# Optimization experiments

Hardware: AMD Instinct MI355X
Metric: run time of the kernel (lower is better)

The kernel has to match this reference:

```python
import jax, jax.numpy as jnp
import numpy as np
import math

B, S, E = 2, 2048, 1024
H, HD = 16, 64
FF = 4 * E
EPS = float(jnp.finfo(jnp.float32).eps)  # torch nn.RMSNorm default eps


def setup_inputs() -> dict:
    key = jax.random.key(0)
    ks = jax.random.split(key, 20)
    sd = 0.02
    inp = {
        "x": jax.random.normal(ks[0], (B, S, E), jnp.float32),
        "wq": jax.random.normal(ks[1], (E, H * HD), jnp.float32) * sd,
        "bq": jnp.zeros((H * HD,), jnp.float32),
        "wk": jax.random.normal(ks[2], (E, HD), jnp.float32) * sd,
        "bk": jnp.zeros((HD,), jnp.float32),
        "wv": jax.random.normal(ks[3], (E, HD), jnp.float32) * sd,
        "bv": jnp.zeros((HD,), jnp.float32),
        "wo": jax.random.normal(ks[4], (H * HD, E), jnp.float32) * sd,
        "bo": jnp.zeros((E,), jnp.float32),
        "wg": jax.random.normal(ks[5], (E, FF), jnp.float32) * sd,
        "bg": jnp.zeros((FF,), jnp.float32),
        "wu": jax.random.normal(ks[6], (E, FF), jnp.float32) * sd,
        "bu": jnp.zeros((FF,), jnp.float32),
        "wd": jax.random.normal(ks[7], (FF, E), jnp.float32) * sd,
        "bd": jnp.zeros((E,), jnp.float32),
        "g1": jnp.ones((E,), jnp.float32),
        "g2": jnp.ones((E,), jnp.float32),
    }
    return inp


def rmsnorm(x, g):
    ms = jnp.mean(jnp.square(x), axis=-1, keepdims=True)
    return x * jax.lax.rsqrt(ms + EPS) * g


def apply_rope(t):
    # t: [B, H, S, D]; llama-style rotate-half, theta=10000, start_pos=0
    d = t.shape[-1]
    half = d // 2
    inv_freq = 1.0 / (10000.0 ** (jnp.arange(half, dtype=jnp.float32) / half))
    pos = jnp.arange(t.shape[2], dtype=jnp.float32)
    ang = pos[:, None] * inv_freq[None, :]  # [S, half]
    cos, sin = jnp.cos(ang), jnp.sin(ang)
    t1, t2 = t[..., :half], t[..., half:]
    return jnp.concatenate([t1 * cos - t2 * sin, t1 * sin + t2 * cos], axis=-1)


def decoder_fwd(x, wq, bq, wk, bk, wv, bv, wo, bo, wg, bg, wu, bu, wd, bd, g1, g2):
    residual = x
    h = rmsnorm(x, g1)
    # MQA projections: H query heads, 1 shared K/V head
    q = (h @ wq + bq).reshape(B, S, H, HD).transpose(0, 2, 1, 3)  # [B,H,S,D]
    k = (h @ wk + bk)[:, None]                                    # [B,1,S,D]
    v = (h @ wv + bv)                                             # [B,S,D]
    q = apply_rope(q)
    k = apply_rope(k)[:, 0]                                       # [B,S,D]
    scores = jnp.einsum("bhqd,bkd->bhqk", q, k) / math.sqrt(HD)
    causal = jnp.tril(jnp.ones((S, S), dtype=bool))
    scores = jnp.where(causal, scores, -jnp.inf)
    attn = jax.nn.softmax(scores, axis=-1)
    out = jnp.einsum("bhqk,bkd->bhqd", attn, v)
    out = out.transpose(0, 2, 1, 3).reshape(B, S, H * HD)
    x = (out @ wo + bo) + residual
    residual = x
    h = rmsnorm(x, g2)
    gated = jax.nn.gelu(h @ wg + bg, approximate=False)  # torch GELU is exact erf
    up = h @ wu + bu
    x = (up * gated) @ wd + bd
    return x + residual


def reference(x, wq, bq, wk, bk, wv, bv, wo, bo, wg, bg, wu, bu, wd, bd, g1, g2):
    return decoder_fwd(x, wq, bq, wk, bk, wv, bv, wo, bo, wg, bg, wu, bu, wd, bd, g1, g2)
```

## Files before the change

### kernel.cpp

```cpp
#include <hip/hip_runtime.h>
#include <hip/hip_bf16.h>
#include <math.h>

#define BB 2
#define SS 2048
#define EE 1024
#define HH 16
#define HD 64
#define FFF 4096
#define MROWS (BB * SS)
#define EPS_F 1.1920929e-7f
#define NQKV 1152

typedef __hip_bfloat16 bf16;
typedef __attribute__((ext_vector_type(8))) short short8;
typedef __attribute__((ext_vector_type(4))) short short4v;
typedef __attribute__((ext_vector_type(4))) float floatx4;

typedef const __attribute__((address_space(1))) void* gas_t;
typedef __attribute__((address_space(3))) void* las_t;

__global__ __launch_bounds__(256) void rmsnorm_kernel(const float* __restrict__ x,
                                                      const float* __restrict__ g,
                                                      bf16* __restrict__ out,
                                                      int cols) {
    int row = blockIdx.x;
    const float* xr = x + (size_t)row * cols;
    float ss = 0.0f;
    for (int c = threadIdx.x; c < cols; c += 256) {
        float v = xr[c];
        ss += v * v;
    }
    for (int off = 32; off > 0; off >>= 1) ss += __shfl_xor(ss, off, 64);
    __shared__ float red[4];
    int wave = threadIdx.x >> 6;
    if ((threadIdx.x & 63) == 0) red[wave] = ss;
    __syncthreads();
    float tot = red[0] + red[1] + red[2] + red[3];
    float rs = rsqrtf(tot / (float)cols + EPS_F);
    bf16* orow = out + (size_t)row * cols;
    for (int c = threadIdx.x; c < cols; c += 256) {
        orow[c] = __float2bfloat16(xr[c] * rs * g[c]);
    }
}

__global__ __launch_bounds__(256) void transpose_cast_kernel(const float* __restrict__ W,
                                                             bf16* __restrict__ Wt,
                                                             int K, int N) {
    __shared__ float t[32][33];
    int n0 = blockIdx.x * 32, k0 = blockIdx.y * 32;
    int tx = threadIdx.x & 31, ty = threadIdx.x >> 5;
#pragma unroll
    for (int i = 0; i < 4; ++i) {
        int kk = ty + i * 8;
        t[kk][tx] = W[(size_t)(k0 + kk) * N + n0 + tx];
    }
    __syncthreads();
#pragma unroll
    for (int i = 0; i < 4; ++i) {
        int nn = ty + i * 8;
        Wt[(size_t)(n0 + nn) * K + k0 + tx] = __float2bfloat16(t[tx][nn]);
    }
}

__global__ __launch_bounds__(256) void pack_bqkv_kernel(const float* __restrict__ bq,
                                                        const float* __restrict__ bk,
                                                        const float* __restrict__ bv,
                                                        float* __restrict__ bqkv) {
    int t = blockIdx.x * 256 + threadIdx.x;
    if (t >= NQKV) return;
    float v;
    if (t < 1024)      v = bq[t];
    else if (t < 1088) v = bk[t - 1024];
    else               v = bv[t - 1088];
    bqkv[t] = v;
}

#define GK 64

__global__ __launch_bounds__(256) void gemm_qkv_kernel(
        const bf16* __restrict__ A, const bf16* __restrict__ Bt,
        const float* __restrict__ bias,
        bf16* __restrict__ qout, float* __restrict__ kvout, int K) {
    __shared__ short As[128 * GK];
    __shared__ short Bs[128 * GK];
    int tid = threadIdx.x;
    int wave = tid >> 6, lane = tid & 63;
    int wm = (wave >> 1) * 64, wn = (wave & 1) * 64;
    int row0 = blockIdx.y * 128, col0 = blockIdx.x * 128;
    int lr = lane & 15, lq = lane >> 4;

    int srow = wave * 32 + (lane >> 3);
    int scol = (lane & 7) * 8;
    const bf16* Abase = A + (size_t)(row0 + srow) * K + scol;
    const bf16* Bbase = Bt + (size_t)(col0 + srow) * K + scol;

    floatx4 acc[4][4];
#pragma unroll
    for (int mi = 0; mi < 4; ++mi)
#pragma unroll
        for (int ni = 0; ni < 4; ++ni)
            acc[mi][ni] = (floatx4){0.f, 0.f, 0.f, 0.f};

    for (int k0 = 0; k0 < K; k0 += GK) {
        __syncthreads();
#pragma unroll
        for (int c = 0; c < 4; ++c) {
            __builtin_amdgcn_global_load_lds(
                (gas_t)(Abase + (size_t)(c * 8) * K + k0),
                (las_t)&As[(wave * 32 + c * 8) * GK], 16, 0, 0);
            __builtin_amdgcn_global_load_lds(
                (gas_t)(Bbase + (size_t)(c * 8) * K + k0),
                (las_t)&Bs[(wave * 32 + c * 8) * GK], 16, 0, 0);
        }
        __syncthreads();
#pragma unroll
        for (int ks = 0; ks < GK; ks += 32) {
            short8 af[4], bfr[4];
#pragma unroll
            for (int mi = 0; mi < 4; ++mi)
                af[mi] = *(const short8*)&As[(wm + mi * 16 + lr) * GK + ks + lq * 8];
#pragma unroll
            for (int ni = 0; ni < 4; ++ni)
                bfr[ni] = *(const short8*)&Bs[(wn + ni * 16 + lr) * GK + ks + lq * 8];
#pragma unroll
            for (int mi = 0; mi < 4; ++mi)
#pragma unroll
                for (int ni = 0; ni < 4; ++ni)
                    acc[mi][ni] = __builtin_amdgcn_mfma_f32_16x16x32_bf16(
                        af[mi], bfr[ni], acc[mi][ni], 0, 0, 0);
        }
    }

#pragma unroll
    for (int mi = 0; mi < 4; ++mi) {
#pragma unroll
        for (int ni = 0; ni < 4; ++ni) {
            int gc = col0 + wn + ni * 16 + lr;
            float bv = bias[gc];
#pragma unroll
            for (int r = 0; r < 4; ++r) {
                int gr = row0 + wm + mi * 16 + lq * 4 + r;
                float c = acc[mi][ni][r] + bv;
                if (gc < 1024) qout[(size_t)gr * 1024 + gc] = __float2bfloat16(c);
                else           kvout[(size_t)gr * 128 + (gc - 1024)] = c;
            }
        }
    }
}

__global__ __launch_bounds__(256) void gemm_n64_kernel(
        const bf16* __restrict__ A, const bf16* __restrict__ Bt,
        const float* __restrict__ bias, const float* __restrict__ aux,
        float* __restrict__ C, int M, int N, int K) {
    __shared__ short As[128 * GK];
    __shared__ short Bs[64 * GK];
    int tid = threadIdx.x;
    int wave = tid >> 6, lane = tid & 63;
    int wm = wave * 32;
    int row0 = blockIdx.y * 128, col0 = blockIdx.x * 64;
    int lr = lane & 15, lq = lane >> 4;

    int srow = (lane >> 3);
    int scol = (lane & 7) * 8;
    const bf16* Abase = A + (size_t)(row0 + wave * 32 + srow) * K + scol;
    const bf16* Bbase = Bt + (size_t)(col0 + wave * 16 + srow) * K + scol;

    floatx4 acc[2][4];
#pragma unroll
    for (int mi = 0; mi < 2; ++mi)
#pragma unroll
        for (int ni = 0; ni < 4; ++ni)
            acc[mi][ni] = (floatx4){0.f, 0.f, 0.f, 0.f};

    for (int k0 = 0; k0 < K; k0 += GK) {
        __syncthreads();
#pragma unroll
        for (int c = 0; c < 4; ++c)
            __builtin_amdgcn_global_load_lds(
                (gas_t)(Abase + (size_t)(c * 8) * K + k0),
                (las_t)&As[(wave * 32 + c * 8) * GK], 16, 0, 0);
#pragma unroll
        for (int c = 0; c < 2; ++c)
            __builtin_amdgcn_global_load_lds(
                (gas_t)(Bbase + (size_t)(c * 8) * K + k0),
                (las_t)&Bs[(wave * 16 + c * 8) * GK], 16, 0, 0);
        __syncthreads();
#pragma unroll
        for (int ks = 0; ks < GK; ks += 32) {
            short8 af[2], bfr[4];
#pragma unroll
            for (int mi = 0; mi < 2; ++mi)
                af[mi] = *(const short8*)&As[(wm + mi * 16 + lr) * GK + ks + lq * 8];
#pragma unroll
            for (int ni = 0; ni < 4; ++ni)
                bfr[ni] = *(const short8*)&Bs[(ni * 16 + lr) * GK + ks + lq * 8];
#pragma unroll
            for (int mi = 0; mi < 2; ++mi)
#pragma unroll
                for (int ni = 0; ni < 4; ++ni)
                    acc[mi][ni] = __builtin_amdgcn_mfma_f32_16x16x32_bf16(
                        af[mi], bfr[ni], acc[mi][ni], 0, 0, 0);
        }
    }

#pragma unroll
    for (int mi = 0; mi < 2; ++mi) {
#pragma unroll
        for (int ni = 0; ni < 4; ++ni) {
            int gc = col0 + ni * 16 + lr;
            float bv = bias[gc];
#pragma unroll
            for (int r = 0; r < 4; ++r) {
                int gr = row0 + wm + mi * 16 + lq * 4 + r;
                size_t idx = (size_t)gr * N + gc;
                C[idx] = acc[mi][ni][r] + bv + aux[idx];
            }
        }
    }
}

__global__ __launch_bounds__(256, 2) void gemm_ffn_kernel(
        const bf16* __restrict__ A, const bf16* __restrict__ Bg,
        const bf16* __restrict__ Bu, const float* __restrict__ biasg,
        const float* __restrict__ biasu, bf16* __restrict__ C, int K) {
    __shared__ short As[128 * GK];
    __shared__ short Gs[128 * GK];
    __shared__ short Us[128 * GK];
    int tid = threadIdx.x;
    int wave = tid >> 6, lane = tid & 63;
    int wm = (wave >> 1) * 64, wn = (wave & 1) * 64;
    int row0 = blockIdx.y * 128, col0 = blockIdx.x * 128;
    int lr = lane & 15, lq = lane >> 4;

    int srow = wave * 32 + (lane >> 3);
    int scol = (lane & 7) * 8;
    const bf16* Abase = A + (size_t)(row0 + srow) * K + scol;
    const bf16* Gbase = Bg + (size_t)(col0 + srow) * K + scol;
    const bf16* Ubase = Bu + (size_t)(col0 + srow) * K + scol;

    floatx4 ag[4][4], au[4][4];
#pragma unroll
    for (int mi = 0; mi < 4; ++mi)
#pragma unroll
        for (int ni = 0; ni < 4; ++ni) {
            ag[mi][ni] = (floatx4){0.f, 0.f, 0.f, 0.f};
            au[mi][ni] = (floatx4){0.f, 0.f, 0.f, 0.f};
        }

    for (int k0 = 0; k0 < K; k0 += GK) {
        __syncthreads();
#pragma unroll
        for (int c = 0; c < 4; ++c) {
            __builtin_amdgcn_global_load_lds(
                (gas_t)(Abase + (size_t)(c * 8) * K + k0),
                (las_t)&As[(wave * 32 + c * 8) * GK], 16, 0, 0);
            __builtin_amdgcn_global_load_lds(
                (gas_t)(Gbase + (size_t)(c * 8) * K + k0),
                (las_t)&Gs[(wave * 32 + c * 8) * GK], 16, 0, 0);
            __builtin_amdgcn_global_load_lds(
                (gas_t)(Ubase + (size_t)(c * 8) * K + k0),
                (las_t)&Us[(wave * 32 + c * 8) * GK], 16, 0, 0);
        }
        __syncthreads();
#pragma unroll
        for (int ks = 0; ks < GK; ks += 32) {
            short8 af[4], gf[4], uf[4];
#pragma unroll
            for (int mi = 0; mi < 4; ++mi)
                af[mi] = *(const short8*)&As[(wm + mi * 16 + lr) * GK + ks + lq * 8];
#pragma unroll
            for (int ni = 0; ni < 4; ++ni) {
                gf[ni] = *(const short8*)&Gs[(wn + ni * 16 + lr) * GK + ks + lq * 8];
                uf[ni] = *(const short8*)&Us[(wn + ni * 16 + lr) * GK + ks + lq * 8];
            }
#pragma unroll
            for (int mi = 0; mi < 4; ++mi)
#pragma unroll
                for (int ni = 0; ni < 4; ++ni) {
                    ag[mi][ni] = __builtin_amdgcn_mfma_f32_16x16x32_bf16(
                        af[mi], gf[ni], ag[mi][ni], 0, 0, 0);
                    au[mi][ni] = __builtin_amdgcn_mfma_f32_16x16x32_bf16(
                        af[mi], uf[ni], au[mi][ni], 0, 0, 0);
                }
        }
    }

#pragma unroll
    for (int mi = 0; mi < 4; ++mi) {
#pragma unroll
        for (int ni = 0; ni < 4; ++ni) {
            int gc = col0 + wn + ni * 16 + lr;
            float bg_ = biasg[gc], bu_ = biasu[gc];
#pragma unroll
            for (int r = 0; r < 4; ++r) {
                int gr = row0 + wm + mi * 16 + lq * 4 + r;
                float g = ag[mi][ni][r] + bg_;
                float u = au[mi][ni][r] + bu_;
                float v = 0.5f * g * (1.0f + erff(g * 0.70710678118654752f)) * u;
                C[(size_t)gr * FFF + gc] = __float2bfloat16(v);
            }
        }
    }
}

__global__ __launch_bounds__(256) void rope_table_kernel(float* __restrict__ ct,
                                                         float* __restrict__ st) {
    int idx = blockIdx.x * 256 + threadIdx.x;
    int i = idx & 31, s = idx >> 5;
    float inv = powf(10000.0f, -(float)i / 32.0f);
    float ang = (float)s * inv;
    ct[idx] = cosf(ang);
    st[idx] = sinf(ang);
}

__global__ __launch_bounds__(256) void rope_q_kernel(bf16* __restrict__ t,
                                                     const float* __restrict__ ct,
                                                     const float* __restrict__ st,
                                                     int total) {
    int idx = blockIdx.x * 256 + threadIdx.x;
    if (idx >= total) return;
    int i = idx & 31;
    int h = (idx >> 5) % HH;
    int row = idx / (32 * HH);
    int s = row & (SS - 1);
    float c = ct[s * 32 + i];
    float sn = st[s * 32 + i];
    size_t base = (size_t)row * (HH * HD) + h * 64 + i;
    float t1 = (float)t[base];
    float t2 = (float)t[base + 32];
    t[base]      = __float2bfloat16((t1 * c - t2 * sn) * 0.125f);
    t[base + 32] = __float2bfloat16((t1 * sn + t2 * c) * 0.125f);
}

__global__ __launch_bounds__(256) void prep_kv_kernel(const float* __restrict__ kv,
                                                      const float* __restrict__ ct,
                                                      const float* __restrict__ st,
                                                      bf16* __restrict__ kbf,
                                                      bf16* __restrict__ vtb) {
    __shared__ float vt[64][65];
    int s0 = blockIdx.x * 64;
    int b  = blockIdx.y;
    int tid = threadIdx.x;

    for (int i = tid; i < 2048; i += 256) {
        int sl = i >> 5, ii = i & 31;
        int s = s0 + sl;
        size_t base = ((size_t)(b * SS + s)) * 128;
        float k1 = kv[base + ii], k2 = kv[base + ii + 32];
        float c = ct[s * 32 + ii];
        float sn = st[s * 32 + ii];
        size_t ob = ((size_t)(b * SS + s)) * 64;
        kbf[ob + ii]      = __float2bfloat16(k1 * c - k2 * sn);
        kbf[ob + ii + 32] = __float2bfloat16(k1 * sn + k2 * c);
    }

    for (int i = tid; i < 4096; i += 256) {
        int s = i >> 6, d = i & 63;
        vt[d][s] = kv[((size_t)(b * SS + s0 + s)) * 128 + 64 + d];
    }
    __syncthreads();
    for (int i = tid; i < 4096; i += 256) {
        int d = i >> 6, sl = i & 63;
        vtb[((size_t)(b * 64 + d)) * SS + s0 + sl] = __float2bfloat16(vt[d][sl]);
    }
}

#define PST 68
#define SM_SHIFT 6.0f

__global__ __launch_bounds__(256, 3) void attn_mfma_kernel(
        const bf16* __restrict__ q, const bf16* __restrict__ kb,
        const bf16* __restrict__ vt,
        float* __restrict__ O0p, float* __restrict__ O1p,
        float* __restrict__ l0p, float* __restrict__ l1p) {
    __shared__ short Kb_s[2][64 * 64];
    __shared__ short Vb_s[2][64 * 64];
    __shared__ short Ps[4][16 * PST];

    int h = blockIdx.y, b = blockIdx.z;
    int px = blockIdx.x >> 1, half = blockIdx.x & 1;
    int tid = threadIdx.x, w = tid >> 6, lane = tid & 63;
    int lr = lane & 15, quad = lane >> 4;
    int rsw = lane & 7;

    float* __restrict__ Op = half ? O1p : O0p;
    float* __restrict__ lp = half ? l1p : l0p;

    const bf16* kbB = kb + (size_t)b * SS * 64;
    const bf16* vtB = vt + (size_t)b * 64 * SS;

    int st_sub = lane >> 3;
    int st_col = ((lane & 7) ^ st_sub) << 3;

    auto stage_tile = [&](int nxt, int j0s) {
#pragma unroll
        for (int i = 0; i < 2; ++i) {
            int rr = i * 32 + w * 8 + st_sub;
            __builtin_amdgcn_global_load_lds(
                (gas_t)(kbB + (size_t)(j0s + rr) * 64 + st_col),
                (las_t)&Kb_s[nxt][(i * 256 + w * 64) * 8], 16, 0, 0);
            __builtin_amdgcn_global_load_lds(
                (gas_t)(vtB + (size_t)rr * SS + j0s + st_col),
                (las_t)&Vb_s[nxt][(i * 256 + w * 64) * 8], 16, 0, 0);
        }
    };

    for (int pass = 0; pass < 2; ++pass) {
        int qt = (pass == 0) ? px : (SS / 64 - 1 - px);
        int q0 = qt * 64;

        const bf16* qrow = q + ((size_t)(b * SS + q0 + w * 16 + lr)) * (HH * HD) + h * HD;
        short8 qf0 = *(const short8*)(qrow + quad * 8);
        short8 qf1 = *(const short8*)(qrow + 32 + quad * 8);

        int n  = qt + 1;
        int n0 = (n + 1) >> 1;
        int tlo = half ? n0 : 0;
        int thi = half ? n  : n0;

        floatx4 O[4];
#pragma unroll
        for (int ni = 0; ni < 4; ++ni) O[ni] = (floatx4){0.f, 0.f, 0.f, 0.f};
        float lrow[4] = {0.f, 0.f, 0.f, 0.f};

        int cur = 0;
        if (tlo < thi) stage_tile(0, tlo * 64);
        __syncthreads();

        for (int t = tlo; t < thi; ++t) {
            if (t + 1 < thi) stage_tile(cur ^ 1, (t + 1) * 64);

            int j0 = t * 64;

            floatx4 S[4];
#pragma unroll
            for (int ni = 0; ni < 4; ++ni) S[ni] = (floatx4){0.f, 0.f, 0.f, 0.f};
#pragma unroll
            for (int ni = 0; ni < 4; ++ni) {
                const short* Kc = &Kb_s[cur][(ni * 16 + lr) * 64];
                short8 b0 = *(const short8*)&Kc[(quad ^ rsw) * 8];
                short8 b1 = *(const short8*)&Kc[((quad ^ rsw) ^ 4) * 8];
                S[ni] = __builtin_amdgcn_mfma_f32_16x16x32_bf16(qf0, b0, S[ni], 0, 0, 0);
                S[ni] = __builtin_amdgcn_mfma_f32_16x16x32_bf16(qf1, b1, S[ni], 0, 0, 0);
            }

            short8 vf[8];
#pragma unroll
            for (int ni = 0; ni < 4; ++ni) {
                const short* Vc = &Vb_s[cur][(ni * 16 + lr) * 64];
                vf[2 * ni]     = *(const short8*)&Vc[(quad ^ rsw) * 8];
                vf[2 * ni + 1] = *(const short8*)&Vc[((quad ^ rsw) ^ 4) * 8];
            }

            if (t == qt) {
                int rowg = q0 + w * 16 + quad * 4;
#pragma unroll
                for (int ni = 0; ni < 4; ++ni) {
                    int colg = j0 + ni * 16 + lr;
#pragma unroll
                    for (int r = 0; r < 4; ++r)
                        if (colg > rowg + r) S[ni][r] = -3.0e38f;
                }
            }

#pragma unroll
            for (int ni = 0; ni < 4; ++ni)
#pragma unroll
                for (int r = 0; r < 4; ++r)
                    S[ni][r] = __expf(S[ni][r] - SM_SHIFT);
#pragma unroll
            for (int r = 0; r < 4; ++r)
                lrow[r] += S[0][r] + S[1][r] + S[2][r] + S[3][r];

#pragma unroll
            for (int ni = 0; ni < 4; ++ni)
#pragma unroll
                for (int r = 0; r < 4; ++r) {
                    bf16 pb = __float2bfloat16(S[ni][r]);
                    Ps[w][(quad * 4 + r) * PST + ni * 16 + lr] = *(short*)&pb;
                }
            short4v a0 = *(const short4v*)&Ps[w][lr * PST + quad * 8];
            short4v a1 = *(const short4v*)&Ps[w][lr * PST + quad * 8 + 4];
            short4v a2 = *(const short4v*)&Ps[w][lr * PST + 32 + quad * 8];
            short4v a3 = *(const short4v*)&Ps[w][lr * PST + 32 + quad * 8 + 4];
            short8 p0 = __builtin_shufflevector(a0, a1, 0, 1, 2, 3, 4, 5, 6, 7);
            short8 p1 = __builtin_shufflevector(a2, a3, 0, 1, 2, 3, 4, 5, 6, 7);

#pragma unroll
            for (int ni = 0; ni < 4; ++ni) {
                O[ni] = __builtin_amdgcn_mfma_f32_16x16x32_bf16(p0, vf[2 * ni], O[ni], 0, 0, 0);
                O[ni] = __builtin_amdgcn_mfma_f32_16x16x32_bf16(p1, vf[2 * ni + 1], O[ni], 0, 0, 0);
            }

            __syncthreads();
            cur ^= 1;
        }

#pragma unroll
        for (int r = 0; r < 4; ++r) {
            float l = lrow[r];
            for (int off = 1; off < 16; off <<= 1) l += __shfl_xor(l, off, 64);
            lrow[r] = l;
        }

#pragma unroll
        for (int ni = 0; ni < 4; ++ni) {
            int gc = h * 64 + ni * 16 + lr;
#pragma unroll
            for (int r = 0; r < 4; ++r) {
                int gr = b * SS + q0 + w * 16 + quad * 4 + r;
                Op[(size_t)gr * (HH * HD) + gc] = O[ni][r];
            }
        }
        if (lr == 0) {
#pragma unroll
            for (int r = 0; r < 4; ++r) {
                int gr = b * SS + q0 + w * 16 + quad * 4 + r;
                lp[(size_t)gr * HH + h] = lrow[r];
            }
        }
    }
}

__global__ __launch_bounds__(256) void attn_combine_kernel(
        const float* __restrict__ O0p, const float* __restrict__ O1p,
        const float* __restrict__ l0p, const float* __restrict__ l1p,
        bf16* __restrict__ o) {
    int idx = blockIdx.x * 256 + threadIdx.x;
    int d4  = idx & 15;
    int hh  = (idx >> 4) & 15;
    int row = idx >> 8;
    float l = l0p[row * HH + hh] + l1p[row * HH + hh];
    float inv = 1.0f / l;
    size_t base = (size_t)row * (HH * HD) + hh * 64 + d4 * 4;
    float4 a = *(const float4*)(O0p + base);
    float4 c = *(const float4*)(O1p + base);
    short4v o4;
    {
        bf16 v0 = __float2bfloat16((a.x + c.x) * inv);
        bf16 v1 = __float2bfloat16((a.y + c.y) * inv);
        bf16 v2 = __float2bfloat16((a.z + c.z) * inv);
        bf16 v3 = __float2bfloat16((a.w + c.w) * inv);
        o4[0] = *(short*)&v0; o4[1] = *(short*)&v1;
        o4[2] = *(short*)&v2; o4[3] = *(short*)&v3;
    }
    *(short4v*)(o + base) = o4;
}

#define MB (1024ull * 1024ull)

extern "C" void kernel_launch(void* const* d_in, const int* in_sizes, int n_in,
                              void* d_out, int out_size, void* d_ws, size_t ws_size,
                              hipStream_t stream) {
    const float* x  = (const float*)d_in[0];
    const float* wq = (const float*)d_in[1];
    const float* bq = (const float*)d_in[2];
    const float* wk = (const float*)d_in[3];
    const float* bk = (const float*)d_in[4];
    const float* wv = (const float*)d_in[5];
    const float* bv = (const float*)d_in[6];
    const float* wo = (const float*)d_in[7];
    const float* bo = (const float*)d_in[8];
    const float* wg = (const float*)d_in[9];
    const float* bg = (const float*)d_in[10];
    const float* wu = (const float*)d_in[11];
    const float* bu = (const float*)d_in[12];
    const float* wd = (const float*)d_in[13];
    const float* bd = (const float*)d_in[14];
    const float* g1 = (const float*)d_in[15];
    const float* g2 = (const float*)d_in[16];
    float* out = (float*)d_out;

    char* ws = (char*)d_ws;
    bf16*  qbf   = (bf16*)(ws);
    bf16*  wuT   = (bf16*)(ws + 8 * MB);
    float* x2    = (float*)(ws + 16 * MB);
    bf16*  h1b   = (bf16*)(ws + 32 * MB);
    float* kv    = (float*)(ws + 40 * MB);
    bf16*  ao    = (bf16*)(ws + 42 * MB);
    bf16*  gg    = (bf16*)(ws + 50 * MB);
    bf16*  kbf   = (bf16*)(ws + 50 * MB);
    bf16*  vtb   = (bf16*)(ws + 50 * MB + 512 * 1024);
    float* Opart0 = (float*)(ws + 16 * MB);
    float* Opart1 = (float*)(ws + 51 * MB);
    float* lpart0 = (float*)(ws + 67 * MB);
    float* lpart1 = (float*)(ws + 67 * MB + 256 * 1024);
    float* ctab   = (float*)(ws + 68 * MB);
    float* stab   = (float*)(ws + 68 * MB + 256 * 1024);
    bf16*  wqkvT = (bf16*)(ws + 82 * MB);
    float* bqkv  = (float*)(ws + 84 * MB + 512 * 1024);
    bf16*  woT   = (bf16*)(ws + 85 * MB);
    bf16*  wgT   = (bf16*)(ws);
    bf16*  wdT   = (bf16*)(ws + 42 * MB);
    bf16*  h2b   = h1b;

    rmsnorm_kernel<<<MROWS, 256, 0, stream>>>(x, g1, h1b, EE);

    transpose_cast_kernel<<<dim3(EE / 32, EE / 32), 256, 0, stream>>>(wq, wqkvT, EE, EE);
    transpose_cast_kernel<<<dim3(HD / 32, EE / 32), 256, 0, stream>>>(wk, wqkvT + (size_t)1024 * EE, EE, HD);
    transpose_cast_kernel<<<dim3(HD / 32, EE / 32), 256, 0, stream>>>(wv, wqkvT + (size_t)1088 * EE, EE, HD);
    pack_bqkv_kernel<<<(NQKV + 255) / 256, 256, 0, stream>>>(bq, bk, bv, bqkv);
    transpose_cast_kernel<<<dim3(EE / 32, EE / 32), 256, 0, stream>>>(wo, woT, EE, EE);

    gemm_qkv_kernel<<<dim3(NQKV / 128, MROWS / 128), 256, 0, stream>>>(
        h1b, wqkvT, bqkv, qbf, kv, EE);

    rope_table_kernel<<<(SS * 32) / 256, 256, 0, stream>>>(ctab, stab);

    {
        int total_q = MROWS * HH * 32;
        rope_q_kernel<<<(total_q + 255) / 256, 256, 0, stream>>>(qbf, ctab, stab, total_q);
    }
    prep_kv_kernel<<<dim3(SS / 64, BB), 256, 0, stream>>>(kv, ctab, stab, kbf, vtb);

    attn_mfma_kernel<<<dim3(2 * SS / 128, HH, BB), 256, 0, stream>>>(
        qbf, kbf, vtb, Opart0, Opart1, lpart0, lpart1);
    attn_combine_kernel<<<(MROWS * HH * HD / 4) / 256, 256, 0, stream>>>(
        Opart0, Opart1, lpart0, lpart1, ao);

    gemm_n64_kernel<<<dim3(EE / 64, MROWS / 128), 256, 0, stream>>>(
        ao, woT, bo, x, x2, MROWS, EE, EE);

    rmsnorm_kernel<<<MROWS, 256, 0, stream>>>(x2, g2, h2b, EE);

    transpose_cast_kernel<<<dim3(FFF / 32, EE / 32), 256, 0, stream>>>(wg, wgT, EE, FFF);
    transpose_cast_kernel<<<dim3(FFF / 32, EE / 32), 256, 0, stream>>>(wu, wuT, EE, FFF);

    gemm_ffn_kernel<<<dim3(FFF / 128, MROWS / 128), 256, 0, stream>>>(
        h2b, wgT, wuT, bg, bu, gg, EE);

    transpose_cast_kernel<<<dim3(EE / 32, FFF / 32), 256, 0, stream>>>(wd, wdT, FFF, EE);
    gemm_n64_kernel<<<dim3(EE / 64, MROWS / 128), 256, 0, stream>>>(
        gg, wdT, bd, x2, out, MROWS, EE, FFF);
}
```

Before: 436.1 us.

## Pipeline FFN gate/up GEMM with double-buffered LDS and widen residual GEMM tiles

```diff
diff --git a/kernel.cpp b/kernel.cpp
--- a/kernel.cpp
+++ b/kernel.cpp
@@ -19,6 +19,11 @@
 
 typedef const __attribute__((address_space(1))) void* gas_t;
 typedef __attribute__((address_space(3))) void* las_t;
+
+#define BAR __builtin_amdgcn_s_barrier()
+#define WLG do { asm volatile("s_waitcnt lgkmcnt(0)" ::: "memory"); \
+                 __builtin_amdgcn_sched_barrier(0); } while (0)
+#define VMC(N) asm volatile("s_waitcnt vmcnt(" #N ")" ::: "memory")
 
 __global__ __launch_bounds__(256) void rmsnorm_kernel(const float* __restrict__ x,
                                                       const float* __restrict__ g,
@@ -149,84 +154,12 @@
     }
 }
 
-__global__ __launch_bounds__(256) void gemm_n64_kernel(
+__global__ __launch_bounds__(256) void gemm_n128_kernel(
         const bf16* __restrict__ A, const bf16* __restrict__ Bt,
         const float* __restrict__ bias, const float* __restrict__ aux,
-        float* __restrict__ C, int M, int N, int K) {
+        float* __restrict__ C, int N, int K) {
     __shared__ short As[128 * GK];
-    __shared__ short Bs[64 * GK];
-    int tid = threadIdx.x;
-    int wave = tid >> 6, lane = tid & 63;
-    int wm = wave * 32;
-    int row0 = blockIdx.y * 128, col0 = blockIdx.x * 64;
-    int lr = lane & 15, lq = lane >> 4;
-
-    int srow = (lane >> 3);
-    int scol = (lane & 7) * 8;
-    const bf16* Abase = A + (size_t)(row0 + wave * 32 + srow) * K + scol;
-    const bf16* Bbase = Bt + (size_t)(col0 + wave * 16 + srow) * K + scol;
-
-    floatx4 acc[2][4];
-#pragma unroll
-    for (int mi = 0; mi < 2; ++mi)
-#pragma unroll
-        for (int ni = 0; ni < 4; ++ni)
-            acc[mi][ni] = (floatx4){0.f, 0.f, 0.f, 0.f};
-
-    for (int k0 = 0; k0 < K; k0 += GK) {
-        __syncthreads();
-#pragma unroll
-        for (int c = 0; c < 4; ++c)
-            __builtin_amdgcn_global_load_lds(
-                (gas_t)(Abase + (size_t)(c * 8) * K + k0),
-                (las_t)&As[(wave * 32 + c * 8) * GK], 16, 0, 0);
-#pragma unroll
-        for (int c = 0; c < 2; ++c)
-            __builtin_amdgcn_global_load_lds(
-                (gas_t)(Bbase + (size_t)(c * 8) * K + k0),
-                (las_t)&Bs[(wave * 16 + c * 8) * GK], 16, 0, 0);
-        __syncthreads();
-#pragma unroll
-        for (int ks = 0; ks < GK; ks += 32) {
-            short8 af[2], bfr[4];
-#pragma unroll
-            for (int mi = 0; mi < 2; ++mi)
-                af[mi] = *(const short8*)&As[(wm + mi * 16 + lr) * GK + ks + lq * 8];
-#pragma unroll
-            for (int ni = 0; ni < 4; ++ni)
-                bfr[ni] = *(const short8*)&Bs[(ni * 16 + lr) * GK + ks + lq * 8];
-#pragma unroll
-            for (int mi = 0; mi < 2; ++mi)
-#pragma unroll
-                for (int ni = 0; ni < 4; ++ni)
-                    acc[mi][ni] = __builtin_amdgcn_mfma_f32_16x16x32_bf16(
-                        af[mi], bfr[ni], acc[mi][ni], 0, 0, 0);
-        }
-    }
-
-#pragma unroll
-    for (int mi = 0; mi < 2; ++mi) {
-#pragma unroll
-        for (int ni = 0; ni < 4; ++ni) {
-            int gc = col0 + ni * 16 + lr;
-            float bv = bias[gc];
-#pragma unroll
-            for (int r = 0; r < 4; ++r) {
-                int gr = row0 + wm + mi * 16 + lq * 4 + r;
-                size_t idx = (size_t)gr * N + gc;
-                C[idx] = acc[mi][ni][r] + bv + aux[idx];
-            }
-        }
-    }
-}
-
-__global__ __launch_bounds__(256, 2) void gemm_ffn_kernel(
-        const bf16* __restrict__ A, const bf16* __restrict__ Bg,
-        const bf16* __restrict__ Bu, const float* __restrict__ biasg,
-        const float* __restrict__ biasu, bf16* __restrict__ C, int K) {
-    __shared__ short As[128 * GK];
-    __shared__ short Gs[128 * GK];
-    __shared__ short Us[128 * GK];
+    __shared__ short Bs[128 * GK];
     int tid = threadIdx.x;
     int wave = tid >> 6, lane = tid & 63;
     int wm = (wave >> 1) * 64, wn = (wave & 1) * 64;
@@ -236,17 +169,14 @@
     int srow = wave * 32 + (lane >> 3);
     int scol = (lane & 7) * 8;
     const bf16* Abase = A + (size_t)(row0 + srow) * K + scol;
-    const bf16* Gbase = Bg + (size_t)(col0 + srow) * K + scol;
-    const bf16* Ubase = Bu + (size_t)(col0 + srow) * K + scol;
-
-    floatx4 ag[4][4], au[4][4];
+    const bf16* Bbase = Bt + (size_t)(col0 + srow) * K + scol;
+
+    floatx4 acc[4][4];
 #pragma unroll
     for (int mi = 0; mi < 4; ++mi)
 #pragma unroll
-        for (int ni = 0; ni < 4; ++ni) {
-            ag[mi][ni] = (floatx4){0.f, 0.f, 0.f, 0.f};
-            au[mi][ni] = (floatx4){0.f, 0.f, 0.f, 0.f};
-        }
+        for (int ni = 0; ni < 4; ++ni)
+            acc[mi][ni] = (floatx4){0.f, 0.f, 0.f, 0.f};
 
     for (int k0 = 0; k0 < K; k0 += GK) {
         __syncthreads();
@@ -256,33 +186,25 @@
                 (gas_t)(Abase + (size_t)(c * 8) * K + k0),
                 (las_t)&As[(wave * 32 + c * 8) * GK], 16, 0, 0);
             __builtin_amdgcn_global_load_lds(
-                (gas_t)(Gbase + (size_t)(c * 8) * K + k0),
-                (las_t)&Gs[(wave * 32 + c * 8) * GK], 16, 0, 0);
-            __builtin_amdgcn_global_load_lds(
-                (gas_t)(Ubase + (size_t)(c * 8) * K + k0),
-                (las_t)&Us[(wave * 32 + c * 8) * GK], 16, 0, 0);
+                (gas_t)(Bbase + (size_t)(c * 8) * K + k0),
+                (las_t)&Bs[(wave * 32 + c * 8) * GK], 16, 0, 0);
         }
         __syncthreads();
 #pragma unroll
         for (int ks = 0; ks < GK; ks += 32) {
-            short8 af[4], gf[4], uf[4];
+            short8 af[4], bfr[4];
 #pragma unroll
             for (int mi = 0; mi < 4; ++mi)
                 af[mi] = *(const short8*)&As[(wm + mi * 16 + lr) * GK + ks + lq * 8];
 #pragma unroll
-            for (int ni = 0; ni < 4; ++ni) {
-                gf[ni] = *(const short8*)&Gs[(wn + ni * 16 + lr) * GK + ks + lq * 8];
-                uf[ni] = *(const short8*)&Us[(wn + ni * 16 + lr) * GK + ks + lq * 8];
-            }
+            for (int ni = 0; ni < 4; ++ni)
+                bfr[ni] = *(const short8*)&Bs[(wn + ni * 16 + lr) * GK + ks + lq * 8];
 #pragma unroll
             for (int mi = 0; mi < 4; ++mi)
 #pragma unroll
-                for (int ni = 0; ni < 4; ++ni) {
-                    ag[mi][ni] = __builtin_amdgcn_mfma_f32_16x16x32_bf16(
-                        af[mi], gf[ni], ag[mi][ni], 0, 0, 0);
-                    au[mi][ni] = __builtin_amdgcn_mfma_f32_16x16x32_bf16(
-                        af[mi], uf[ni], au[mi][ni], 0, 0, 0);
-                }
+                for (int ni = 0; ni < 4; ++ni)
+                    acc[mi][ni] = __builtin_amdgcn_mfma_f32_16x16x32_bf16(
+                        af[mi], bfr[ni], acc[mi][ni], 0, 0, 0);
         }
     }
 
@@ -291,10 +213,133 @@
 #pragma unroll
         for (int ni = 0; ni < 4; ++ni) {
             int gc = col0 + wn + ni * 16 + lr;
-            float bg_ = biasg[gc], bu_ = biasu[gc];
+            float bv = bias[gc];
 #pragma unroll
             for (int r = 0; r < 4; ++r) {
                 int gr = row0 + wm + mi * 16 + lq * 4 + r;
+                size_t idx = (size_t)gr * N + gc;
+                C[idx] = acc[mi][ni][r] + bv + aux[idx];
+            }
+        }
+    }
+}
+
+#define FFN_RD(KH, MH) \
+    short8 af[4], gf[2], uf[2]; \
+    { const short* Ap = &Ab[buf][KH][0]; const short* Bp = &Bb[buf][KH][0]; \
+      af[0] = *(const short8*)&Ap[(wr * 128 + ((MH) * 4 + 0) * 16 + lr) * 32 + quad * 8]; \
+      af[1] = *(const short8*)&Ap[(wr * 128 + ((MH) * 4 + 1) * 16 + lr) * 32 + quad * 8]; \
+      af[2] = *(const short8*)&Ap[(wr * 128 + ((MH) * 4 + 2) * 16 + lr) * 32 + quad * 8]; \
+      af[3] = *(const short8*)&Ap[(wr * 128 + ((MH) * 4 + 3) * 16 + lr) * 32 + quad * 8]; \
+      gf[0] = *(const short8*)&Bp[(wc * 32 + lr) * 32 + quad * 8]; \
+      gf[1] = *(const short8*)&Bp[(wc * 32 + 16 + lr) * 32 + quad * 8]; \
+      uf[0] = *(const short8*)&Bp[4096 + (wc * 32 + lr) * 32 + quad * 8]; \
+      uf[1] = *(const short8*)&Bp[4096 + (wc * 32 + 16 + lr) * 32 + quad * 8]; }
+
+#define FFN_MM(MH) \
+    __builtin_amdgcn_s_setprio(1); \
+    { _Pragma("unroll") for (int mi = 0; mi < 4; ++mi) { \
+        ag[(MH) * 4 + mi][0] = __builtin_amdgcn_mfma_f32_16x16x32_bf16(af[mi], gf[0], ag[(MH) * 4 + mi][0], 0, 0, 0); \
+        ag[(MH) * 4 + mi][1] = __builtin_amdgcn_mfma_f32_16x16x32_bf16(af[mi], gf[1], ag[(MH) * 4 + mi][1], 0, 0, 0); \
+        au[(MH) * 4 + mi][0] = __builtin_amdgcn_mfma_f32_16x16x32_bf16(af[mi], uf[0], au[(MH) * 4 + mi][0], 0, 0, 0); \
+        au[(MH) * 4 + mi][1] = __builtin_amdgcn_mfma_f32_16x16x32_bf16(af[mi], uf[1], au[(MH) * 4 + mi][1], 0, 0, 0); } } \
+    __builtin_amdgcn_s_setprio(0);
+
+__global__ __launch_bounds__(512, 2) void gemm_ffn_kernel(
+        const bf16* __restrict__ A, const bf16* __restrict__ Bg,
+        const bf16* __restrict__ Bu, const float* __restrict__ biasg,
+        const float* __restrict__ biasu, bf16* __restrict__ C, int K) {
+    __shared__ short Ab[2][2][8192];
+    __shared__ short Bb[2][2][8192];
+
+    const int tid = threadIdx.x;
+    const int w = tid >> 6, lane = tid & 63;
+    const int wr = w >> 2, wc = w & 3;
+    const int lr = lane & 15, quad = lane >> 4;
+    const int row0 = blockIdx.y * 256, col0 = blockIdx.x * 128;
+    const int NT = K >> 6;
+
+    const int sr = tid >> 2;
+    const int sc = (tid & 3) * 8;
+
+    auto stageA = [&](short* dst, int kcol) {
+        __builtin_amdgcn_global_load_lds(
+            (gas_t)(A + (size_t)(row0 + sr) * K + kcol + sc),
+            (las_t)(dst + tid * 8), 16, 0, 0);
+        __builtin_amdgcn_global_load_lds(
+            (gas_t)(A + (size_t)(row0 + 128 + sr) * K + kcol + sc),
+            (las_t)(dst + 4096 + tid * 8), 16, 0, 0);
+    };
+    auto stageB = [&](short* dst, int kcol) {
+        __builtin_amdgcn_global_load_lds(
+            (gas_t)(Bg + (size_t)(col0 + sr) * K + kcol + sc),
+            (las_t)(dst + tid * 8), 16, 0, 0);
+        __builtin_amdgcn_global_load_lds(
+            (gas_t)(Bu + (size_t)(col0 + sr) * K + kcol + sc),
+            (las_t)(dst + 4096 + tid * 8), 16, 0, 0);
+    };
+
+    floatx4 ag[8][2], au[8][2];
+#pragma unroll
+    for (int mi = 0; mi < 8; ++mi)
+#pragma unroll
+        for (int ni = 0; ni < 2; ++ni) {
+            ag[mi][ni] = (floatx4){0.f, 0.f, 0.f, 0.f};
+            au[mi][ni] = (floatx4){0.f, 0.f, 0.f, 0.f};
+        }
+
+    stageA(&Ab[0][0][0], 0);
+    stageB(&Bb[0][0][0], 0);
+    stageA(&Ab[0][1][0], 32);
+    stageB(&Bb[0][1][0], 32);
+    stageA(&Ab[1][0][0], 64);
+    stageB(&Bb[1][0][0], 64);
+    VMC(8);
+    BAR;
+
+    for (int k = 0; k < NT; ++k) {
+        const int buf = k & 1;
+        {
+            FFN_RD(0, 0)
+            if (k + 1 < NT) stageA(&Ab[buf ^ 1][1][0], (k + 1) * 64 + 32);
+            BAR; WLG;
+            FFN_MM(0)
+            BAR;
+        }
+        {
+            FFN_RD(0, 1)
+            if (k + 1 < NT) stageB(&Bb[buf ^ 1][1][0], (k + 1) * 64 + 32);
+            BAR; WLG;
+            FFN_MM(1)
+            if (k < NT - 1) { VMC(8); } else { VMC(0); }
+            BAR;
+        }
+        {
+            FFN_RD(1, 0)
+            if (k + 2 < NT) stageA(&Ab[buf][0][0], (k + 2) * 64);
+            BAR; WLG;
+            FFN_MM(0)
+            BAR;
+        }
+        {
+            FFN_RD(1, 1)
+            if (k + 2 < NT) stageB(&Bb[buf][0][0], (k + 2) * 64);
+            BAR; WLG;
+            FFN_MM(1)
+            if (k < NT - 2) { VMC(8); } else if (k == NT - 2) { VMC(4); }
+            BAR;
+        }
+    }
+
+#pragma unroll
+    for (int mi = 0; mi < 8; ++mi) {
+#pragma unroll
+        for (int ni = 0; ni < 2; ++ni) {
+            int gc = col0 + wc * 32 + ni * 16 + lr;
+            float bg_ = biasg[gc], bu_ = biasu[gc];
+#pragma unroll
+            for (int r = 0; r < 4; ++r) {
+                int gr = row0 + wr * 128 + mi * 16 + quad * 4 + r;
                 float g = ag[mi][ni][r] + bg_;
                 float u = au[mi][ni][r] + bu_;
                 float v = 0.5f * g * (1.0f + erff(g * 0.70710678118654752f)) * u;
@@ -619,18 +664,18 @@
     attn_combine_kernel<<<(MROWS * HH * HD / 4) / 256, 256, 0, stream>>>(
         Opart0, Opart1, lpart0, lpart1, ao);
 
-    gemm_n64_kernel<<<dim3(EE / 64, MROWS / 128), 256, 0, stream>>>(
-        ao, woT, bo, x, x2, MROWS, EE, EE);
+    gemm_n128_kernel<<<dim3(EE / 128, MROWS / 128), 256, 0, stream>>>(
+        ao, woT, bo, x, x2, EE, EE);
 
     rmsnorm_kernel<<<MROWS, 256, 0, stream>>>(x2, g2, h2b, EE);
 
     transpose_cast_kernel<<<dim3(FFF / 32, EE / 32), 256, 0, stream>>>(wg, wgT, EE, FFF);
     transpose_cast_kernel<<<dim3(FFF / 32, EE / 32), 256, 0, stream>>>(wu, wuT, EE, FFF);
 
-    gemm_ffn_kernel<<<dim3(FFF / 128, MROWS / 128), 256, 0, stream>>>(
+    gemm_ffn_kernel<<<dim3(FFF / 128, MROWS / 256), 512, 0, stream>>>(
         h2b, wgT, wuT, bg, bu, gg, EE);
 
     transpose_cast_kernel<<<dim3(EE / 32, FFF / 32), 256, 0, stream>>>(wd, wdT, FFF, EE);
-    gemm_n64_kernel<<<dim3(EE / 64, MROWS / 128), 256, 0, stream>>>(
-        gg, wdT, bd, x2, out, MROWS, EE, FFF);
-}
+    gemm_n128_kernel<<<dim3(EE / 128, MROWS / 128), 256, 0, stream>>>(
+        gg, wdT, bd, x2, out, EE, FFF);
+}
```

After: 461.4 us. 5.8% more time.
